# Performance work log

Measured on AMD Instinct MI355X. Metric: run time of the kernel, lower is better.

Reference implementation:

```python
import jax, jax.numpy as jnp
import numpy as np

N = 100000          # num nodes
E = 3200000         # num edges (avg degree 32)
G = 64              # num graphs in batch
F_IN = 2            # num_node_features
H = 16              # hidden_size
NUM_LAYERS = 2


def sage_conv(x, src, dst, W_l, b_l, W_r):
    # PyG SAGEConv (mean aggr): out = lin_l(mean_{j in N(i)} x_j) + lin_r(x_i)
    msg = x[src]                                                  # [E, F] gather
    agg = jax.ops.segment_sum(msg, dst, num_segments=N)          # [N, F] scatter-add
    deg = jax.ops.segment_sum(jnp.ones((src.shape[0],), x.dtype), dst, num_segments=N)
    mean = agg / jnp.maximum(deg, 1.0)[:, None]
    return mean @ W_l + b_l + x @ W_r


def setup_inputs() -> dict:
    key = jax.random.key(0)
    ks = jax.random.split(key, 10)
    x = jax.random.normal(ks[0], (N, F_IN), dtype=jnp.float32)
    edge_index = jax.random.randint(ks[1], (2, E), 0, N, dtype=jnp.int64)
    batch = jnp.sort(jax.random.randint(ks[2], (N,), 0, G, dtype=jnp.int64))
    s1 = 1.0 / np.sqrt(F_IN)
    s2 = 1.0 / np.sqrt(H)
    return {
        "x": x,
        "edge_index": edge_index,
        "batch": batch,
        "W1_l": jax.random.uniform(ks[3], (F_IN, H), jnp.float32, -s1, s1),
        "b1_l": jnp.zeros((H,), jnp.float32),
        "W1_r": jax.random.uniform(ks[4], (F_IN, H), jnp.float32, -s1, s1),
        "W2_l": jax.random.uniform(ks[5], (H, H), jnp.float32, -s2, s2),
        "b2_l": jnp.zeros((H,), jnp.float32),
        "W2_r": jax.random.uniform(ks[6], (H, H), jnp.float32, -s2, s2),
        "W_end": jax.random.uniform(ks[7], (H, 1), jnp.float32, -s2, s2),
        "b_end": jnp.zeros((1,), jnp.float32),
    }


def reference(x, edge_index, batch, W1_l, b1_l, W1_r, W2_l, b2_l, W2_r, W_end, b_end):
    src, dst = edge_index[0], edge_index[1]
    h = sage_conv(x, src, dst, W1_l, b1_l, W1_r)                 # conv1
    for _ in range(NUM_LAYERS - 1):
        h = jax.nn.relu(h)
        h = sage_conv(h, src, dst, W2_l, b2_l, W2_r)             # conv2
    h = jax.nn.relu(h)
    # dropout is identity in eval mode
    h = h @ W_end + b_end                                         # [N, 1]
    # global mean pool over graphs
    summed = jax.ops.segment_sum(h, batch, num_segments=G)       # [G, 1]
    counts = jax.ops.segment_sum(jnp.ones((N,), h.dtype), batch, num_segments=G)
    pooled = summed / jnp.maximum(counts, 1.0)[:, None]
    return jax.nn.sigmoid(pooled)                                 # [G, 1]
```

## Files before the change

### kernel.cpp

```cpp
#include <hip/hip_runtime.h>
#include <math.h>

#define NN 100000
#define NE 3200000
#define NG 64
#define HID 16
#define EPB 8192
#define NBLKE ((NE + EPB - 1) / EPB)
#define NBUCK ((NN + 255) / 256)
#define LMAX 10240
#define MAXB 10240

typedef unsigned int uint;
typedef float vf2 __attribute__((ext_vector_type(2)));
typedef int   vi4 __attribute__((ext_vector_type(4)));


template <bool HI>
__device__ inline vf2 dec2fp8(uint u) {
#if __has_builtin(__builtin_amdgcn_cvt_pk_f32_fp8)
    return __builtin_amdgcn_cvt_pk_f32_fp8((int)u, HI);
#else
    vf2 r;
    uint b0 = (u >> (HI ? 16 : 0)) & 0xff;
    uint b1 = (u >> (HI ? 24 : 8)) & 0xff;
    uint em0 = b0 & 0x7f, em1 = b1 & 0x7f;
    float v0 = (em0 >= 8) ? __uint_as_float(((em0 >> 3) + 120) << 23 | (em0 & 7) << 20)
                          : (float)em0 * 0.001953125f;
    float v1 = (em1 >= 8) ? __uint_as_float(((em1 >> 3) + 120) << 23 | (em1 & 7) << 20)
                          : (float)em1 * 0.001953125f;
    r.x = (b0 & 0x80) ? -v0 : v0;
    r.y = (b1 & 0x80) ? -v1 : v1;
    return r;
#endif
}

__device__ inline uint enc1fp8(float f) {
    if (!(f > 0.f)) return 0u;
    f = fminf(f, 448.f);
    uint b = __float_as_uint(f);
    int e = (int)(b >> 23) - 127;
    if (e >= -6) {
        uint m = b & 0x7fffffu;
        uint r = (m + 0x7ffffu + ((m >> 20) & 1u)) >> 20;
        uint code = ((uint)(e + 7) << 3) + r;
        return code > 126u ? 126u : code;
    }
    float t = f * 512.f;
    return (uint)(t + 0.5f);
}

template <bool HI>
__device__ inline uint packfp8x2(float a, float b, uint old) {
#if __has_builtin(__builtin_amdgcn_cvt_pk_fp8_f32)
    return (uint)__builtin_amdgcn_cvt_pk_fp8_f32(a, b, (int)old, HI);
#else
    uint v = enc1fp8(a) | (enc1fp8(b) << 8);
    return HI ? ((old & 0x0000ffffu) | (v << 16)) : ((old & 0xffff0000u) | v);
#endif
}

__global__ __launch_bounds__(512) void k_sortblk(const int* __restrict__ src,
                                                 const int* __restrict__ dst,
                                                 int* __restrict__ blockCnt,
                                                 int* __restrict__ pairs,
                                                 float* __restrict__ gsum,
                                                 float* __restrict__ gcnt) {
    __shared__ int hist[NBUCK];
    __shared__ int s[512];
    __shared__ int cur[NBUCK];
    int t = threadIdx.x, blk = blockIdx.x;
    if (blk == 0 && t < NG) { gsum[t] = 0.f; gcnt[t] = 0.f; }
    for (int i = t; i < NBUCK; i += 512) hist[i] = 0;
    __syncthreads();
    int base = blk * EPB;
    int nE = min(EPB, NE - base);
    int n4 = nE >> 2;
    const vi4* d4 = (const vi4*)(dst + base);
    const vi4* s4 = (const vi4*)(src + base);
    for (int i = t; i < n4; i += 512) {
        vi4 v = d4[i];
        atomicAdd(&hist[v.x >> 8], 1);
        atomicAdd(&hist[v.y >> 8], 1);
        atomicAdd(&hist[v.z >> 8], 1);
        atomicAdd(&hist[v.w >> 8], 1);
    }
    __syncthreads();
    s[t] = (t < NBUCK) ? hist[t] : 0;
    __syncthreads();
    for (int off = 1; off < 512; off <<= 1) {
        int x = s[t] + ((t >= off) ? s[t - off] : 0);
        __syncthreads();
        s[t] = x;
        __syncthreads();
    }
    int row = blk * (NBUCK + 1);
    if (t < NBUCK) {
        int excl = t ? s[t - 1] : 0;
        blockCnt[row + t] = excl;
        cur[t] = excl;
    }
    if (t == 0) blockCnt[row + NBUCK] = nE;
    __syncthreads();
    for (int i = t; i < n4; i += 512) {
        vi4 dv = d4[i];
        vi4 sv = s4[i];
        int p0 = atomicAdd(&cur[dv.x >> 8], 1);
        pairs[base + p0] = (sv.x << 8) | (dv.x & 255);
        int p1 = atomicAdd(&cur[dv.y >> 8], 1);
        pairs[base + p1] = (sv.y << 8) | (dv.y & 255);
        int p2 = atomicAdd(&cur[dv.z >> 8], 1);
        pairs[base + p2] = (sv.z << 8) | (dv.z & 255);
        int p3 = atomicAdd(&cur[dv.w >> 8], 1);
        pairs[base + p3] = (sv.w << 8) | (dv.w & 255);
    }
}

__global__ __launch_bounds__(512) void k_fill2c1(
    const int* __restrict__ blockCnt, const int* __restrict__ pairs,
    const float* __restrict__ x,
    const float* __restrict__ W1l, const float* __restrict__ b1l,
    const float* __restrict__ W1r,
    int* __restrict__ nodeOff, int* __restrict__ nodeCnt,
    int* __restrict__ csr, uint* __restrict__ h8) {
    __shared__ int segS[NBLKE];
    __shared__ int lofs[NBLKE + 1];
    __shared__ int s[512];
    __shared__ int a[256];
    __shared__ int lcur[256];
    __shared__ int lpair[LMAX];
    int t = threadIdx.x, b = blockIdx.x;
    int segc = 0;
    if (t < NBLKE) {
        int row = t * (NBUCK + 1);
        int o0 = blockCnt[row + b];
        int o1 = blockCnt[row + b + 1];
        segS[t] = t * EPB + o0;
        segc = o1 - o0;
    }
    if (t < 256) a[t] = 0;
    s[t] = (t < NBLKE) ? segc : 0;
    __syncthreads();
    for (int off = 1; off < 512; off <<= 1) {
        int v = s[t] + ((t >= off) ? s[t - off] : 0);
        __syncthreads();
        s[t] = v;
        __syncthreads();
    }
    if (t < NBLKE) lofs[t] = t ? s[t - 1] : 0;
    if (t == 0) lofs[NBLKE] = s[511];
    __syncthreads();
    int tot = lofs[NBLKE];
    if (t < NBLKE) {
        int bl = lofs[t];
        int gs = segS[t];
        for (int j = 0; j < segc; ++j) {
            int v = pairs[gs + j];
            if (bl + j < LMAX) lpair[bl + j] = v;
            atomicAdd(&a[v & 255], 1);
        }
    }
    __syncthreads();
    for (int off = 1; off < 256; off <<= 1) {
        int v = 0;
        if (t < 256) v = a[t] + ((t >= off) ? a[t - off] : 0);
        __syncthreads();
        if (t < 256) a[t] = v;
        __syncthreads();
    }
    if (t < 256) lcur[t] = t ? a[t - 1] : 0;
    __syncthreads();
    int cbase = b * MAXB;
    for (int idx = t; idx < tot; idx += 512) {
        int v;
        if (idx < LMAX) {
            v = lpair[idx];
        } else {
            int lo = 0, hi = NBLKE - 1;
            while (lo < hi) {
                int mid = (lo + hi + 1) >> 1;
                if (lofs[mid] <= idx) lo = mid; else hi = mid - 1;
            }
            v = pairs[segS[lo] + idx - lofs[lo]];
        }
        int pos = atomicAdd(&lcur[v & 255], 1);
        csr[cbase + pos] = v >> 8;
    }
    __syncthreads();
    if (t < 256) {
        int node = b * 256 + t;
        if (node < NN) {
            int excl = t ? a[t - 1] : 0;
            int cntn = a[t] - excl;
            nodeOff[node] = cbase + excl;
            nodeCnt[node] = cntn;
            float s0 = 0.f, s1 = 0.f;
            int gb = cbase + excl;
            for (int k = 0; k < cntn; ++k) {
                int sv = csr[gb + k];
                float2 xv = *(const float2*)(x + 2 * sv);
                s0 += xv.x; s1 += xv.y;
            }
            float inv = 1.0f / fmaxf((float)cntn, 1.0f);
            float m0 = s0 * inv, m1 = s1 * inv;
            float x0 = x[2 * node], x1 = x[2 * node + 1];
            float o[16];
#pragma unroll
            for (int h = 0; h < 16; ++h)
                o[h] = fmaxf(m0 * W1l[h] + m1 * W1l[16 + h] + b1l[h]
                           + x0 * W1r[h] + x1 * W1r[16 + h], 0.f);
            uint4 w;
            w.x = packfp8x2<false>(o[0],  o[1],  0u);
            w.x = packfp8x2<true >(o[2],  o[3],  w.x);
            w.y = packfp8x2<false>(o[4],  o[5],  0u);
            w.y = packfp8x2<true >(o[6],  o[7],  w.y);
            w.z = packfp8x2<false>(o[8],  o[9],  0u);
            w.z = packfp8x2<true >(o[10], o[11], w.z);
            w.w = packfp8x2<false>(o[12], o[13], 0u);
            w.w = packfp8x2<true >(o[14], o[15], w.w);
            *(uint4*)(h8 + (size_t)node * 4) = w;
        }
    }
}

__global__ __launch_bounds__(256) void k_conv2pool(
    const int* __restrict__ nodeOff, const int* __restrict__ nodeCnt,
    const int* __restrict__ csr, const uint* __restrict__ h8,
    const float* __restrict__ W2l, const float* __restrict__ b2l,
    const float* __restrict__ W2r, const float* __restrict__ Wend,
    const float* __restrict__ bend, const int* __restrict__ batch,
    float* __restrict__ gsum, float* __restrict__ gcnt) {
    __shared__ float sWl[256], sWr[256], sB[HID], sWe[HID];
    __shared__ float sm[64][17], shr[64][17];
    __shared__ float ls[NG], lc[NG];
    int t = threadIdx.x;
    sWl[t] = W2l[t];
    sWr[t] = W2r[t];
    if (t < HID) { sB[t] = b2l[t]; sWe[t] = Wend[t]; }
    if (t < NG) { ls[t] = 0.f; lc[t] = 0.f; }

    int g = t >> 2;
    int l4 = t & 3;
    int gbase = (t & 63) & 60;
    int i = blockIdx.x * 64 + g;
    int beg = 0, end = 0;
    if (i < NN) { beg = nodeOff[i]; end = beg + nodeCnt[i]; }
    float a0 = 0.f, a1 = 0.f, a2 = 0.f, a3 = 0.f;
    int kb = beg;
    uint ub[8];
    for (; kb + 8 <= end; kb += 8) {
        int sv0 = csr[kb + l4];
        int sv1 = csr[kb + 4 + l4];
#pragma unroll
        for (int j = 0; j < 4; ++j) {
            int s = __shfl(sv0, gbase + j, 64);
            ub[j] = h8[(size_t)s * 4 + l4];
        }
#pragma unroll
        for (int j = 0; j < 4; ++j) {
            int s = __shfl(sv1, gbase + j, 64);
            ub[4 + j] = h8[(size_t)s * 4 + l4];
        }
#pragma unroll
        for (int j = 0; j < 8; ++j) {
            vf2 p0 = dec2fp8<false>(ub[j]);
            vf2 p1 = dec2fp8<true >(ub[j]);
            a0 += p0.x; a1 += p0.y; a2 += p1.x; a3 += p1.y;
        }
    }
    for (; kb + 4 <= end; kb += 4) {
        int sv = csr[kb + l4];
#pragma unroll
        for (int j = 0; j < 4; ++j) {
            int s = __shfl(sv, gbase + j, 64);
            ub[j] = h8[(size_t)s * 4 + l4];
        }
#pragma unroll
        for (int j = 0; j < 4; ++j) {
            vf2 p0 = dec2fp8<false>(ub[j]);
            vf2 p1 = dec2fp8<true >(ub[j]);
            a0 += p0.x; a1 += p0.y; a2 += p1.x; a3 += p1.y;
        }
    }
    if (kb < end) {
        int idx = kb + l4;
        int sv = (idx < end) ? csr[idx] : 0;
        int nb = end - kb;
        for (int j = 0; j < nb; ++j) {
            int s = __shfl(sv, gbase + j, 64);
            uint u = h8[(size_t)s * 4 + l4];
            vf2 p0 = dec2fp8<false>(u);
            vf2 p1 = dec2fp8<true >(u);
            a0 += p0.x; a1 += p0.y; a2 += p1.x; a3 += p1.y;
        }
    }
    if (i < NN) {
        float inv = 1.0f / fmaxf((float)(end - beg), 1.0f);
        uint us = h8[(size_t)i * 4 + l4];
        vf2 q0 = dec2fp8<false>(us);
        vf2 q1 = dec2fp8<true >(us);
        sm[g][4 * l4 + 0] = a0 * inv;
        sm[g][4 * l4 + 1] = a1 * inv;
        sm[g][4 * l4 + 2] = a2 * inv;
        sm[g][4 * l4 + 3] = a3 * inv;
        shr[g][4 * l4 + 0] = q0.x;
        shr[g][4 * l4 + 1] = q0.y;
        shr[g][4 * l4 + 2] = q1.x;
        shr[g][4 * l4 + 3] = q1.y;
    }
    __syncthreads();

    float y = 0.f;
    if (i < NN) {
#pragma unroll
        for (int k = 0; k < 4; ++k) {
            int h = 4 * l4 + k;
            float a = sB[h];
#pragma unroll
            for (int f = 0; f < HID; ++f)
                a += sm[g][f] * sWl[f * HID + h] + shr[g][f] * sWr[f * HID + h];
            y += fmaxf(a, 0.f) * sWe[h];
        }
    }
    y += __shfl_xor(y, 1, 64);
    y += __shfl_xor(y, 2, 64);
    if (l4 == 0 && i < NN) {
        int bg = batch[i];
        atomicAdd(&ls[bg], y + bend[0]);
        atomicAdd(&lc[bg], 1.0f);
    }
    __syncthreads();
    if (t < NG && lc[t] != 0.0f) {
        unsafeAtomicAdd(&gsum[t], ls[t]);
        unsafeAtomicAdd(&gcnt[t], lc[t]);
    }
}

__global__ void k_final(const float* __restrict__ gsum, const float* __restrict__ gcnt,
                        float* __restrict__ out) {
    int g = threadIdx.x;
    if (g < NG) {
        float p = gsum[g] / fmaxf(gcnt[g], 1.0f);
        out[g] = 1.0f / (1.0f + expf(-p));
    }
}

extern "C" void kernel_launch(void* const* d_in, const int* in_sizes, int n_in,
                              void* d_out, int out_size, void* d_ws, size_t ws_size,
                              hipStream_t stream) {
    const float* x    = (const float*)d_in[0];
    const int*   ei   = (const int*)d_in[1];
    const int*   batch= (const int*)d_in[2];
    const float* W1l  = (const float*)d_in[3];
    const float* b1l  = (const float*)d_in[4];
    const float* W1r  = (const float*)d_in[5];
    const float* W2l  = (const float*)d_in[6];
    const float* b2l  = (const float*)d_in[7];
    const float* W2r  = (const float*)d_in[8];
    const float* Wend = (const float*)d_in[9];
    const float* bend = (const float*)d_in[10];

    const int* src = ei;
    const int* dst = ei + NE;

    float* gsum      = (float*)d_ws;
    float* gcnt      = (float*)d_ws + NG;
    int*   blockCnt  = (int*)d_ws + 2 * NG;
    int*   nodeOff   = blockCnt + (size_t)NBLKE * (NBUCK + 1);
    int*   nodeCnt   = nodeOff + NN;
    size_t po        = (size_t)(nodeCnt + NN - (int*)d_ws);
    po               = (po + 3) & ~(size_t)3;
    int*   pairs     = (int*)d_ws + po;
    int*   csr       = pairs + NE;
    uint*  h8        = (uint*)(csr + (size_t)NBUCK * MAXB);

    k_sortblk   <<<NBLKE, 512, 0, stream>>>(src, dst, blockCnt, pairs, gsum, gcnt);
    k_fill2c1   <<<NBUCK, 512, 0, stream>>>(blockCnt, pairs, x, W1l, b1l, W1r,
                                            nodeOff, nodeCnt, csr, h8);
    k_conv2pool <<<(NN + 63) / 64, 256, 0, stream>>>(nodeOff, nodeCnt, csr, h8,
                                                     W2l, b2l, W2r, Wend, bend,
                                                     batch, gsum, gcnt);
    k_final     <<<1, 64, 0, stream>>>(gsum, gcnt, (float*)d_out);
}
```

Measured before the change: 121.2 us.

## Split bucket fill across two blocks and parallelize segment copy and neighbor sums

```diff
diff --git a/kernel.cpp b/kernel.cpp
--- a/kernel.cpp
+++ b/kernel.cpp
@@ -129,7 +129,10 @@
     __shared__ int a[256];
     __shared__ int lcur[256];
     __shared__ int lpair[LMAX];
-    int t = threadIdx.x, b = blockIdx.x;
+    __shared__ float ps0[512], ps1[512];
+    int t = threadIdx.x;
+    int b = blockIdx.x >> 1;
+    int half = blockIdx.x & 1;
     int segc = 0;
     if (t < NBLKE) {
         int row = t * (NBUCK + 1);
@@ -151,14 +154,29 @@
     if (t == 0) lofs[NBLKE] = s[511];
     __syncthreads();
     int tot = lofs[NBLKE];
-    if (t < NBLKE) {
-        int bl = lofs[t];
-        int gs = segS[t];
-        for (int j = 0; j < segc; ++j) {
-            int v = pairs[gs + j];
-            if (bl + j < LMAX) lpair[bl + j] = v;
-            atomicAdd(&a[v & 255], 1);
-        }
+    {
+        int gid = t >> 3, lane = t & 7;
+        for (int sg = gid; sg < NBLKE; sg += 64) {
+            int bl = lofs[sg];
+            int sc = lofs[sg + 1] - bl;
+            int gs = segS[sg];
+            for (int j = lane; j < sc; j += 8) {
+                int pos = bl + j;
+                if (pos < LMAX) lpair[pos] = pairs[gs + j];
+            }
+        }
+    }
+    __syncthreads();
+    int totL = min(tot, LMAX);
+    for (int idx = t; idx < totL; idx += 512)
+        atomicAdd(&a[lpair[idx] & 255], 1);
+    for (int idx = LMAX + t; idx < tot; idx += 512) {
+        int lo = 0, hi = NBLKE - 1;
+        while (lo < hi) {
+            int mid = (lo + hi + 1) >> 1;
+            if (lofs[mid] <= idx) lo = mid; else hi = mid - 1;
+        }
+        atomicAdd(&a[pairs[segS[lo] + idx - lofs[lo]] & 255], 1);
     }
     __syncthreads();
     for (int off = 1; off < 256; off <<= 1) {
@@ -171,38 +189,56 @@
     if (t < 256) lcur[t] = t ? a[t - 1] : 0;
     __syncthreads();
     int cbase = b * MAXB;
-    for (int idx = t; idx < tot; idx += 512) {
-        int v;
-        if (idx < LMAX) {
-            v = lpair[idx];
-        } else {
-            int lo = 0, hi = NBLKE - 1;
-            while (lo < hi) {
-                int mid = (lo + hi + 1) >> 1;
-                if (lofs[mid] <= idx) lo = mid; else hi = mid - 1;
-            }
-            v = pairs[segS[lo] + idx - lofs[lo]];
-        }
-        int pos = atomicAdd(&lcur[v & 255], 1);
-        csr[cbase + pos] = v >> 8;
-    }
-    __syncthreads();
-    if (t < 256) {
-        int node = b * 256 + t;
+    for (int idx = t; idx < totL; idx += 512) {
+        int v = lpair[idx];
+        int dl = v & 255;
+        if ((dl >> 7) == half) {
+            int pos = atomicAdd(&lcur[dl], 1);
+            csr[cbase + pos] = v >> 8;
+        }
+    }
+    for (int idx = LMAX + t; idx < tot; idx += 512) {
+        int lo = 0, hi = NBLKE - 1;
+        while (lo < hi) {
+            int mid = (lo + hi + 1) >> 1;
+            if (lofs[mid] <= idx) lo = mid; else hi = mid - 1;
+        }
+        int v = pairs[segS[lo] + idx - lofs[lo]];
+        int dl = v & 255;
+        if ((dl >> 7) == half) {
+            int pos = atomicAdd(&lcur[dl], 1);
+            csr[cbase + pos] = v >> 8;
+        }
+    }
+    __syncthreads();
+    {
+        int local = t >> 2, q = t & 3;
+        int dl = half * 128 + local;
+        int excl = dl ? a[dl - 1] : 0;
+        int cntn = a[dl] - excl;
+        int gb = cbase + excl;
+        float s0 = 0.f, s1 = 0.f;
+        for (int k = q; k < cntn; k += 4) {
+            int sv = csr[gb + k];
+            float2 xv = *(const float2*)(x + 2 * sv);
+            s0 += xv.x; s1 += xv.y;
+        }
+        ps0[t] = s0; ps1[t] = s1;
+    }
+    __syncthreads();
+    if (t < 128) {
+        int dl = half * 128 + t;
+        int node = b * 256 + dl;
         if (node < NN) {
-            int excl = t ? a[t - 1] : 0;
-            int cntn = a[t] - excl;
+            int excl = dl ? a[dl - 1] : 0;
+            int cntn = a[dl] - excl;
             nodeOff[node] = cbase + excl;
             nodeCnt[node] = cntn;
-            float s0 = 0.f, s1 = 0.f;
-            int gb = cbase + excl;
-            for (int k = 0; k < cntn; ++k) {
-                int sv = csr[gb + k];
-                float2 xv = *(const float2*)(x + 2 * sv);
-                s0 += xv.x; s1 += xv.y;
-            }
+            int p4 = t * 4;
+            float m0 = ps0[p4] + ps0[p4 + 1] + ps0[p4 + 2] + ps0[p4 + 3];
+            float m1 = ps1[p4] + ps1[p4 + 1] + ps1[p4 + 2] + ps1[p4 + 3];
             float inv = 1.0f / fmaxf((float)cntn, 1.0f);
-            float m0 = s0 * inv, m1 = s1 * inv;
+            m0 *= inv; m1 *= inv;
             float x0 = x[2 * node], x1 = x[2 * node + 1];
             float o[16];
 #pragma unroll
@@ -375,8 +411,8 @@
     uint*  h8        = (uint*)(csr + (size_t)NBUCK * MAXB);
 
     k_sortblk   <<<NBLKE, 512, 0, stream>>>(src, dst, blockCnt, pairs, gsum, gcnt);
-    k_fill2c1   <<<NBUCK, 512, 0, stream>>>(blockCnt, pairs, x, W1l, b1l, W1r,
-                                            nodeOff, nodeCnt, csr, h8);
+    k_fill2c1   <<<2 * NBUCK, 512, 0, stream>>>(blockCnt, pairs, x, W1l, b1l, W1r,
+                                                nodeOff, nodeCnt, csr, h8);
     k_conv2pool <<<(NN + 63) / 64, 256, 0, stream>>>(nodeOff, nodeCnt, csr, h8,
                                                      W2l, b2l, W2r, Wend, bend,
                                                      batch, gsum, gcnt);
```

Measured after the change: 116.3 us. -4.1%, faster.
